# Kernel optimization log

Measured on AMD Instinct MI355X. Metric: run time of the kernel, lower is better.

The kernel has to match this reference:

```python
import jax, jax.numpy as jnp
import numpy as np

B, D, DEPTH, C = 8192, 2048, 10, 1000
NUM_INNER = 2 ** DEPTH - 1   # 1023
NUM_LEAVES = 2 ** DEPTH      # 1024


def setup_inputs() -> dict:
    key = jax.random.key(0)
    k1, k2, k3, k4 = jax.random.split(key, 4)
    x = jax.random.normal(k1, (B, D), dtype=jnp.float32)
    # scale weights like a typical init so sigmoid isn't fully saturated
    W = jax.random.normal(k2, (D, NUM_INNER), dtype=jnp.float32) * 0.02
    b = jax.random.normal(k3, (NUM_INNER,), dtype=jnp.float32) * 0.02
    leaf_dist = jax.random.normal(k4, (NUM_LEAVES, C), dtype=jnp.float32)
    return {"x": x, "W": W, "b": b, "leaf_dist": leaf_dist}


def reference(x, W, b, leaf_dist):
    # inner node routing probabilities: [B, num_inner]
    decisions = jax.nn.sigmoid(x @ W + b)
    depth = int(np.log2(decisions.shape[1] + 1))
    pp = jnp.ones((x.shape[0], 1), dtype=x.dtype)  # path probs, starts at root
    for d in range(depth):  # small fixed loop over tree depth
        s, e = 2 ** d - 1, 2 ** (d + 1) - 1
        ld = decisions[:, s:e]                      # [B, 2^d]
        pp = jnp.concatenate([pp * ld, pp * (1.0 - ld)], axis=1)  # [B, 2^(d+1)]
        # faithful reproduction of the original's even/odd reordering
        pp = jnp.concatenate([pp[:, ::2], pp[:, 1::2]], axis=1)
    leaf_probs = jax.nn.softmax(leaf_dist, axis=1)  # [num_leaves, C]
    return pp @ leaf_probs                          # [B, C]
```

## Files before the change

kernel.cpp:

```cpp
#include <hip/hip_runtime.h>

typedef __attribute__((ext_vector_type(8))) unsigned short ushort8v;
typedef __attribute__((ext_vector_type(8))) __bf16 bf16x8;
typedef __attribute__((ext_vector_type(4))) float floatx4;

__device__ __forceinline__ unsigned short f2b(float f) {
    unsigned u = __float_as_uint(f);
    unsigned r = u + 0x7fffu + ((u >> 16) & 1u);
    return (unsigned short)(r >> 16);
}
__device__ __forceinline__ float b2f(unsigned short h) {
    return __uint_as_float(((unsigned)h) << 16);
}

__device__ __forceinline__ void gload16(const unsigned short* g, unsigned short* l) {
    __builtin_amdgcn_global_load_lds(
        (const __attribute__((address_space(1))) unsigned int*)g,
        (__attribute__((address_space(3))) unsigned int*)l,
        16, 0, 0);
}


__global__ __launch_bounds__(256) void prep_kernel(const float* __restrict__ x,
                                                   unsigned short* __restrict__ A2x,
                                                   const float* __restrict__ W,
                                                   unsigned short* __restrict__ B2w,
                                                   const float* __restrict__ ld_,
                                                   unsigned short* __restrict__ B2p) {
    __shared__ float tile[32 * 33];
    __shared__ float buf[1000];
    __shared__ float red[8];
    const int b = blockIdx.x, t = threadIdx.x;
    if (b < 2048) {
        const int mt = b >> 2, kq = (b & 3) * 64;
        const int kco = t >> 4, l16 = t & 15;
        const float* xr0 = x + (size_t)(mt * 16 + l16) * 2048;
#pragma unroll
        for (int i = 0; i < 4; i++) {
            const int kc = kq + i * 16 + kco;
            const float* xr = xr0 + kc * 8;
            float4 v0 = *(const float4*)xr;
            float4 v1 = *(const float4*)(xr + 4);
            ushort8v o;
            o[0] = f2b(v0.x); o[1] = f2b(v0.y); o[2] = f2b(v0.z); o[3] = f2b(v0.w);
            o[4] = f2b(v1.x); o[5] = f2b(v1.y); o[6] = f2b(v1.z); o[7] = f2b(v1.w);
            *(ushort8v*)(A2x + ((size_t)(mt * 256 + kc) * 16 + l16) * 8) = o;
        }
    } else if (b < 4096) {
        const int idx = b - 2048;
        const int n0 = (idx & 31) * 32, k0 = (idx >> 5) * 32;
        const int tx = t & 31, ty = t >> 5;
#pragma unroll
        for (int i = 0; i < 4; i++) {
            int k = k0 + ty + i * 8, n = n0 + tx;
            tile[(ty + i * 8) * 33 + tx] = (n < 1023) ? W[(size_t)k * 1023 + n] : 0.f;
        }
        __syncthreads();
#pragma unroll
        for (int i = 0; i < 4; i++) {
            int n = n0 + ty + i * 8, k = k0 + tx;
            size_t off = ((size_t)((n >> 4) * 256 + (k >> 3)) * 16 + (n & 15)) * 8 + (k & 7);
            B2w[off] = f2b(tile[tx * 33 + ty + i * 8]);
        }
    } else {
        const int l0 = b - 4096;
        const float* r = ld_ + (size_t)l0 * 1000;
        float mx = -3.4e38f;
        for (int i = t; i < 1000; i += 256) { float v = r[i]; buf[i] = v; mx = fmaxf(mx, v); }
#pragma unroll
        for (int o = 32; o > 0; o >>= 1) mx = fmaxf(mx, __shfl_down(mx, o));
        if ((t & 63) == 0) red[t >> 6] = mx;
        __syncthreads();
        mx = fmaxf(fmaxf(red[0], red[1]), fmaxf(red[2], red[3]));
        float s = 0.f;
        for (int i = t; i < 1000; i += 256) { float e = __expf(buf[i] - mx); buf[i] = e; s += e; }
#pragma unroll
        for (int o = 32; o > 0; o >>= 1) s += __shfl_down(s, o);
        if ((t & 63) == 0) red[4 + (t >> 6)] = s;
        __syncthreads();
        float inv = 1.f / (red[4] + red[5] + red[6] + red[7]);
        for (int i = t; i < 1024; i += 256) {
            float pv = (i < 1000) ? buf[i] * inv : 0.f;
            size_t off = ((size_t)((i >> 4) * 128 + (l0 >> 3)) * 16 + (i & 15)) * 8 + (l0 & 7);
            B2p[off] = f2b(pv);
        }
    }
}

__global__ __launch_bounds__(256) void pp_kernel(const unsigned short* __restrict__ dec,
                                                 unsigned short* __restrict__ A2p) {
    __shared__ unsigned short dsh[8 * 1024];
    __shared__ float pa[8 * 1024];
    __shared__ float pb[8 * 1024];
    const int t = threadIdx.x;
    const int r0 = blockIdx.x * 8;
    {
        const ushort8v* src = (const ushort8v*)(dec + (size_t)r0 * 1024);
        ushort8v* dst = (ushort8v*)dsh;
        for (int g = t; g < 1024; g += 256) dst[g] = src[g];
    }
    if (t < 8) pa[t * 1024] = 1.f;
    __syncthreads();
    float* cur = pa; float* nxt = pb;
    for (int dep = 0; dep < 10; dep++) {
        const int half = 1 << dep;
        const int len  = half << 1;
        const int total = len << 3;
        for (int idx = t; idx < total; idx += 256) {
            const int r = idx >> (dep + 1);
            const int j = idx & (len - 1);
            int tt = j >> dep;
            int s  = j & (half - 1);
            int i2 = 2 * s + tt;
            int u  = i2 >> dep;
            int rr = i2 & (half - 1);
            float dv = b2f(dsh[r * 1024 + half - 1 + rr]);
            nxt[r * 1024 + j] = cur[r * 1024 + rr] * (u ? (1.f - dv) : dv);
        }
        __syncthreads();
        float* tmp = cur; cur = nxt; nxt = tmp;
    }
    for (int i = t; i < 8192; i += 256) {
        const int r = i >> 10, j = i & 1023;
        const int rrow = r0 + r;
        size_t off = ((size_t)((rrow >> 4) * 128 + (j >> 3)) * 16 + (rrow & 15)) * 8 + (j & 7);
        A2p[off] = f2b(cur[r * 1024 + j]);
    }
}

#define VMW(N) asm volatile("s_waitcnt vmcnt(" #N ")" ::: "memory")

#define P5_STEP(ks_, b_, VM_, DOSTAGE_)                                           \
    {                                                                             \
        VMW(VM_);                                                                 \
        __builtin_amdgcn_s_barrier();                                             \
        __builtin_amdgcn_sched_barrier(0);                                        \
        const unsigned short* lA = &lds[(b_)][0];                                 \
        const unsigned short* lB = &lds[(b_)][8192];                              \
        bf16x8 af[4], bv[4];                                                      \
        _Pragma("unroll")                                                         \
        for (int m2 = 0; m2 < 4; m2++)                                            \
            af[m2] = __builtin_bit_cast(bf16x8,                                   \
                *(const ushort8v*)&lA[(wr * 4 + m2) * 512 + quad * 128 + l16 * 8]); \
        _Pragma("unroll")                                                         \
        for (int n2 = 0; n2 < 4; n2++)                                            \
            bv[n2] = __builtin_bit_cast(bf16x8,                                   \
                *(const ushort8v*)&lB[(wc * 4 + n2) * 512 + quad * 128 + l16 * 8]); \
        asm volatile("s_waitcnt lgkmcnt(0)" ::: "memory");                        \
        __builtin_amdgcn_sched_barrier(0);                                        \
        __builtin_amdgcn_s_barrier();                                             \
        __builtin_amdgcn_sched_barrier(0);                                        \
        if (DOSTAGE_) STAGE((ks_) + 5, (b_));                                     \
        __builtin_amdgcn_s_setprio(1);                                            \
        _Pragma("unroll")                                                         \
        for (int m2 = 0; m2 < 4; m2++)                                            \
            _Pragma("unroll")                                                     \
            for (int n2 = 0; n2 < 4; n2++)                                        \
                acc[m2][n2] = __builtin_amdgcn_mfma_f32_16x16x32_bf16(            \
                    af[m2], bv[n2], acc[m2][n2], 0, 0, 0);                        \
        __builtin_amdgcn_s_setprio(0);                                            \
    }

template <int EPI, int KC>
__global__ __launch_bounds__(512, 2) void gemm_p5(const unsigned short* __restrict__ A2,
                                                  const unsigned short* __restrict__ B2,
                                                  const float* __restrict__ bias,
                                                  unsigned short* __restrict__ obf,
                                                  float* __restrict__ of32, int ldo) {
    __shared__ unsigned short lds[5][12288];

    const int tid  = threadIdx.x;
    const int lane = tid & 63;
    const int wave = tid >> 6;
    const int quad = lane >> 4, l16 = lane & 15;
    const int wr = wave >> 1, wc = wave & 1;

    const int bid = blockIdx.x;
    const int xcd = bid & 7;
    const int j   = bid >> 3;
    const int bm  = xcd * 4 + (j & 3);
    const int bn  = j >> 2;

    const unsigned short* gA0 = A2 + ((size_t)(bm * 16 + wave * 2)     * KC + quad) * 128 + l16 * 8;
    const unsigned short* gA1 = A2 + ((size_t)(bm * 16 + wave * 2 + 1) * KC + quad) * 128 + l16 * 8;
    const unsigned short* gB0 = B2 + ((size_t)(bn * 8  + wave)         * KC + quad) * 128 + l16 * 8;
    const int dA0 = (wave * 8 + quad) * 128 + l16 * 8;
    const int dA1 = dA0 + 512;
    const int dB0 = 8192 + (wave * 4 + quad) * 128 + l16 * 8;

    floatx4 acc[4][4] = {};
    constexpr int nks = KC / 4;

    auto STAGE = [&](int ks, int b) {
        const size_t ko = (size_t)ks * 512;
        gload16(gA0 + ko, &lds[b][dA0]);
        gload16(gA1 + ko, &lds[b][dA1]);
        gload16(gB0 + ko, &lds[b][dB0]);
    };

    STAGE(0, 0); STAGE(1, 1); STAGE(2, 2); STAGE(3, 3); STAGE(4, 4);

    int bb = 0;
    for (int ks = 0; ks < nks - 5; ++ks) {
        P5_STEP(ks, bb, 12, true);
        bb = (bb == 4) ? 0 : bb + 1;
    }
    P5_STEP(nks - 5, (nks - 5) % 5, 12, false);
    P5_STEP(nks - 4, (nks - 4) % 5, 9,  false);
    P5_STEP(nks - 3, (nks - 3) % 5, 6,  false);
    P5_STEP(nks - 2, (nks - 2) % 5, 3,  false);
    P5_STEP(nks - 1, (nks - 1) % 5, 0,  false);

    const int mt0 = bm * 16 + wr * 4;
    const int nt0 = bn * 8  + wc * 4;
#pragma unroll
    for (int n2 = 0; n2 < 4; n2++) {
        const int col = (nt0 + n2) * 16 + l16;
        float bbias = 0.f;
        if constexpr (EPI == 0) bbias = (col < 1023) ? bias[col] : 0.f;
#pragma unroll
        for (int m2 = 0; m2 < 4; m2++) {
            const int row0 = (mt0 + m2) * 16 + quad * 4;
#pragma unroll
            for (int r = 0; r < 4; r++) {
                float v = acc[m2][n2][r];
                if constexpr (EPI == 0) {
                    float sgm = 1.f / (1.f + __expf(-(v + bbias)));
                    obf[(size_t)(row0 + r) * ldo + col] = f2b(sgm);
                } else {
                    if (col < 1000) of32[(size_t)(row0 + r) * ldo + col] = v;
                }
            }
        }
    }
}

extern "C" void kernel_launch(void* const* d_in, const int* in_sizes, int n_in,
                              void* d_out, int out_size, void* d_ws, size_t ws_size,
                              hipStream_t stream) {
    const float* x   = (const float*)d_in[0];
    const float* W   = (const float*)d_in[1];
    const float* b   = (const float*)d_in[2];
    const float* ldd = (const float*)d_in[3];
    float* out = (float*)d_out;

    char* ws = (char*)d_ws;
    unsigned short* A2x = (unsigned short*)(ws);
    unsigned short* A2p = (unsigned short*)(ws);
    unsigned short* B2w = (unsigned short*)(ws + 33554432);
    unsigned short* dec = (unsigned short*)(ws + 37748736);
    unsigned short* B2p = (unsigned short*)(ws + 54525952);

    prep_kernel<<<5120, 256, 0, stream>>>(x, A2x, W, B2w, ldd, B2p);
    gemm_p5<0, 256><<<256, 512, 0, stream>>>(A2x, B2w, b, dec, nullptr, 1024);
    pp_kernel<<<1024, 256, 0, stream>>>(dec, A2p);
    gemm_p5<1, 128><<<256, 512, 0, stream>>>(A2p, B2p, nullptr, nullptr, out, 1000);
}
```

Baseline: 209.1 us.

## Shrink GEMM tiles to 128x128 with 4 waves and a 4-stage pipeline

Both GEMMs move from 256x128 output tiles on 8 waves with a 5-deep LDS ring to 128x128 tiles on 4 waves with a 4-deep ring, which doubles the grid to 512 blocks. The staging address math is rewritten so each thread issues four 16-byte loads, and the XCD-aware block swizzle is dropped for a plain bn-fastest mapping. The aim is more blocks per CU and a smaller LDS footprint for better occupancy and load balance. In exchange, arithmetic intensity per tile drops, global and L2 traffic rises, and the L2 locality from the swizzle is lost.

```diff
diff --git a/kernel.cpp b/kernel.cpp
--- a/kernel.cpp
+++ b/kernel.cpp
@@ -130,44 +130,44 @@
 
 #define VMW(N) asm volatile("s_waitcnt vmcnt(" #N ")" ::: "memory")
 
-#define P5_STEP(ks_, b_, VM_, DOSTAGE_)                                           \
-    {                                                                             \
-        VMW(VM_);                                                                 \
-        __builtin_amdgcn_s_barrier();                                             \
-        __builtin_amdgcn_sched_barrier(0);                                        \
-        const unsigned short* lA = &lds[(b_)][0];                                 \
-        const unsigned short* lB = &lds[(b_)][8192];                              \
-        bf16x8 af[4], bv[4];                                                      \
-        _Pragma("unroll")                                                         \
-        for (int m2 = 0; m2 < 4; m2++)                                            \
-            af[m2] = __builtin_bit_cast(bf16x8,                                   \
-                *(const ushort8v*)&lA[(wr * 4 + m2) * 512 + quad * 128 + l16 * 8]); \
-        _Pragma("unroll")                                                         \
-        for (int n2 = 0; n2 < 4; n2++)                                            \
-            bv[n2] = __builtin_bit_cast(bf16x8,                                   \
-                *(const ushort8v*)&lB[(wc * 4 + n2) * 512 + quad * 128 + l16 * 8]); \
-        asm volatile("s_waitcnt lgkmcnt(0)" ::: "memory");                        \
-        __builtin_amdgcn_sched_barrier(0);                                        \
-        __builtin_amdgcn_s_barrier();                                             \
-        __builtin_amdgcn_sched_barrier(0);                                        \
-        if (DOSTAGE_) STAGE((ks_) + 5, (b_));                                     \
-        __builtin_amdgcn_s_setprio(1);                                            \
-        _Pragma("unroll")                                                         \
-        for (int m2 = 0; m2 < 4; m2++)                                            \
-            _Pragma("unroll")                                                     \
-            for (int n2 = 0; n2 < 4; n2++)                                        \
-                acc[m2][n2] = __builtin_amdgcn_mfma_f32_16x16x32_bf16(            \
-                    af[m2], bv[n2], acc[m2][n2], 0, 0, 0);                        \
-        __builtin_amdgcn_s_setprio(0);                                            \
+#define P4_STEP(ks_, b_, VM_, DOSTAGE_)                                             \
+    {                                                                               \
+        VMW(VM_);                                                                   \
+        __builtin_amdgcn_s_barrier();                                               \
+        __builtin_amdgcn_sched_barrier(0);                                          \
+        const unsigned short* lA = &lds[(b_)][0];                                   \
+        const unsigned short* lB = &lds[(b_)][4096];                                \
+        bf16x8 af[4], bv[4];                                                        \
+        _Pragma("unroll")                                                           \
+        for (int m2 = 0; m2 < 4; m2++)                                              \
+            af[m2] = __builtin_bit_cast(bf16x8,                                     \
+                *(const ushort8v*)&lA[((wr * 4 + m2) * 4 + quad) * 128 + l16 * 8]); \
+        _Pragma("unroll")                                                           \
+        for (int n2 = 0; n2 < 4; n2++)                                              \
+            bv[n2] = __builtin_bit_cast(bf16x8,                                     \
+                *(const ushort8v*)&lB[((wc * 4 + n2) * 4 + quad) * 128 + l16 * 8]); \
+        asm volatile("s_waitcnt lgkmcnt(0)" ::: "memory");                          \
+        __builtin_amdgcn_sched_barrier(0);                                          \
+        __builtin_amdgcn_s_barrier();                                               \
+        __builtin_amdgcn_sched_barrier(0);                                          \
+        if (DOSTAGE_) STAGE((ks_) + 4, (b_));                                       \
+        __builtin_amdgcn_s_setprio(1);                                              \
+        _Pragma("unroll")                                                           \
+        for (int m2 = 0; m2 < 4; m2++)                                              \
+            _Pragma("unroll")                                                       \
+            for (int n2 = 0; n2 < 4; n2++)                                          \
+                acc[m2][n2] = __builtin_amdgcn_mfma_f32_16x16x32_bf16(              \
+                    af[m2], bv[n2], acc[m2][n2], 0, 0, 0);                          \
+        __builtin_amdgcn_s_setprio(0);                                              \
     }
 
 template <int EPI, int KC>
-__global__ __launch_bounds__(512, 2) void gemm_p5(const unsigned short* __restrict__ A2,
+__global__ __launch_bounds__(256, 2) void gemm_p4(const unsigned short* __restrict__ A2,
                                                   const unsigned short* __restrict__ B2,
                                                   const float* __restrict__ bias,
                                                   unsigned short* __restrict__ obf,
                                                   float* __restrict__ of32, int ldo) {
-    __shared__ unsigned short lds[5][12288];
+    __shared__ unsigned short lds[4][8192];
 
     const int tid  = threadIdx.x;
     const int lane = tid & 63;
@@ -176,17 +176,19 @@
     const int wr = wave >> 1, wc = wave & 1;
 
     const int bid = blockIdx.x;
-    const int xcd = bid & 7;
-    const int j   = bid >> 3;
-    const int bm  = xcd * 4 + (j & 3);
-    const int bn  = j >> 2;
-
-    const unsigned short* gA0 = A2 + ((size_t)(bm * 16 + wave * 2)     * KC + quad) * 128 + l16 * 8;
-    const unsigned short* gA1 = A2 + ((size_t)(bm * 16 + wave * 2 + 1) * KC + quad) * 128 + l16 * 8;
-    const unsigned short* gB0 = B2 + ((size_t)(bn * 8  + wave)         * KC + quad) * 128 + l16 * 8;
-    const int dA0 = (wave * 8 + quad) * 128 + l16 * 8;
-    const int dA1 = dA0 + 512;
-    const int dB0 = 8192 + (wave * 4 + quad) * 128 + l16 * 8;
+    const int bn  = bid & 7;
+    const int bm  = bid >> 3;
+
+    const int c0  = tid >> 4;
+    const int sub = (tid & 15) * 8;
+    const unsigned short* gA0 = A2 + ((size_t)(bm * 8 + (c0 >> 2))        * KC + (c0 & 3)) * 128 + sub;
+    const unsigned short* gA1 = A2 + ((size_t)(bm * 8 + ((c0 + 16) >> 2)) * KC + (c0 & 3)) * 128 + sub;
+    const unsigned short* gB0 = B2 + ((size_t)(bn * 8 + (c0 >> 2))        * KC + (c0 & 3)) * 128 + sub;
+    const unsigned short* gB1 = B2 + ((size_t)(bn * 8 + ((c0 + 16) >> 2)) * KC + (c0 & 3)) * 128 + sub;
+    const int dA0 = c0 * 128 + sub;
+    const int dA1 = (c0 + 16) * 128 + sub;
+    const int dB0 = 4096 + c0 * 128 + sub;
+    const int dB1 = 4096 + (c0 + 16) * 128 + sub;
 
     floatx4 acc[4][4] = {};
     constexpr int nks = KC / 4;
@@ -196,23 +198,21 @@
         gload16(gA0 + ko, &lds[b][dA0]);
         gload16(gA1 + ko, &lds[b][dA1]);
         gload16(gB0 + ko, &lds[b][dB0]);
+        gload16(gB1 + ko, &lds[b][dB1]);
     };
 
-    STAGE(0, 0); STAGE(1, 1); STAGE(2, 2); STAGE(3, 3); STAGE(4, 4);
-
-    int bb = 0;
-    for (int ks = 0; ks < nks - 5; ++ks) {
-        P5_STEP(ks, bb, 12, true);
-        bb = (bb == 4) ? 0 : bb + 1;
-    }
-    P5_STEP(nks - 5, (nks - 5) % 5, 12, false);
-    P5_STEP(nks - 4, (nks - 4) % 5, 9,  false);
-    P5_STEP(nks - 3, (nks - 3) % 5, 6,  false);
-    P5_STEP(nks - 2, (nks - 2) % 5, 3,  false);
-    P5_STEP(nks - 1, (nks - 1) % 5, 0,  false);
-
-    const int mt0 = bm * 16 + wr * 4;
-    const int nt0 = bn * 8  + wc * 4;
+    STAGE(0, 0); STAGE(1, 1); STAGE(2, 2); STAGE(3, 3);
+
+    for (int ks = 0; ks < nks - 4; ++ks) {
+        P4_STEP(ks, ks & 3, 12, true);
+    }
+    P4_STEP(nks - 4, (nks - 4) & 3, 12, false);
+    P4_STEP(nks - 3, (nks - 3) & 3, 8,  false);
+    P4_STEP(nks - 2, (nks - 2) & 3, 4,  false);
+    P4_STEP(nks - 1, (nks - 1) & 3, 0,  false);
+
+    const int mt0 = bm * 8 + wr * 4;
+    const int nt0 = bn * 8 + wc * 4;
 #pragma unroll
     for (int n2 = 0; n2 < 4; n2++) {
         const int col = (nt0 + n2) * 16 + l16;
@@ -252,7 +252,7 @@
     unsigned short* B2p = (unsigned short*)(ws + 54525952);
 
     prep_kernel<<<5120, 256, 0, stream>>>(x, A2x, W, B2w, ldd, B2p);
-    gemm_p5<0, 256><<<256, 512, 0, stream>>>(A2x, B2w, b, dec, nullptr, 1024);
+    gemm_p4<0, 256><<<512, 256, 0, stream>>>(A2x, B2w, b, dec, nullptr, 1024);
     pp_kernel<<<1024, 256, 0, stream>>>(dec, A2p);
-    gemm_p5<1, 128><<<256, 512, 0, stream>>>(A2p, B2p, nullptr, nullptr, out, 1000);
-}
+    gemm_p4<1, 128><<<512, 256, 0, stream>>>(A2p, B2p, nullptr, nullptr, out, 1000);
+}
```

After: 210.3 us. Within noise of the previous version (+0.6%).
